# Optimization experiments

Measured on AMD Instinct MI355X. Metric: run time of the kernel, lower is better.

The kernel has to match this reference:

```python
import jax, jax.numpy as jnp
import numpy as np

DEPTH = 4
HEADS = 8
DIM = 512
HID = 1024  # int(512 * 2.0)
P = 16
IMG = 224
GRID = IMG // P          # 14
NPATCH = GRID * GRID     # 196
NTOK = NPATCH + 1        # 197 (cls token)
BATCH = 64
EPS = 1e-5               # torch LayerNorm default


def layernorm(x, w, b):
    mu = jnp.mean(x, axis=-1, keepdims=True)
    var = jnp.mean(jnp.square(x - mu), axis=-1, keepdims=True)
    return (x - mu) * jax.lax.rsqrt(var + EPS) * w + b


def setup_inputs() -> dict:
    key = jax.random.key(0)
    ks = jax.random.split(key, 12)
    s = 0.02
    inp = {
        "x": jax.random.normal(ks[0], (BATCH, 3, IMG, IMG), jnp.float32),
        # patch-embed conv as matmul: kernel flattened in torch order (c, kh, kw)
        "conv_w": jax.random.normal(ks[1], (3 * P * P, DIM), jnp.float32) * s,
        "conv_b": jnp.zeros((DIM,), jnp.float32),
        "cls_token": jax.random.normal(ks[2], (1, 1, DIM), jnp.float32) * s,
        "pos_embed": jax.random.normal(ks[3], (1, NTOK, DIM), jnp.float32) * s,
        # per-block params stacked along depth
        "ln1_w": jnp.ones((DEPTH, DIM), jnp.float32),
        "ln1_b": jnp.zeros((DEPTH, DIM), jnp.float32),
        "qkv_w": jax.random.normal(ks[4], (DEPTH, DIM, 3 * DIM), jnp.float32) * s,
        "qkv_b": jnp.zeros((DEPTH, 3 * DIM), jnp.float32),
        "proj_w": jax.random.normal(ks[5], (DEPTH, DIM, DIM), jnp.float32) * s,
        "proj_b": jnp.zeros((DEPTH, DIM), jnp.float32),
        "ln2_w": jnp.ones((DEPTH, DIM), jnp.float32),
        "ln2_b": jnp.zeros((DEPTH, DIM), jnp.float32),
        "fc1_w": jax.random.normal(ks[6], (DEPTH, DIM, HID), jnp.float32) * s,
        "fc1_b": jnp.zeros((DEPTH, HID), jnp.float32),
        "fc2_w": jax.random.normal(ks[7], (DEPTH, HID, DIM), jnp.float32) * s,
        "fc2_b": jnp.zeros((DEPTH, DIM), jnp.float32),
        "norm_w": jnp.ones((DIM,), jnp.float32),
        "norm_b": jnp.zeros((DIM,), jnp.float32),
    }
    return inp


def reference(x, conv_w, conv_b, cls_token, pos_embed,
              ln1_w, ln1_b, qkv_w, qkv_b, proj_w, proj_b,
              ln2_w, ln2_b, fc1_w, fc1_b, fc2_w, fc2_b,
              norm_w, norm_b):
    B = x.shape[0]
    hd = DIM // HEADS
    scale = hd ** -0.5
    # PatchEmbed: conv with kernel=stride=patch == patch extraction + matmul
    patches = x.reshape(B, 3, GRID, P, GRID, P)
    patches = patches.transpose(0, 2, 4, 1, 3, 5).reshape(B, NPATCH, 3 * P * P)
    tok = patches @ conv_w + conv_b                      # [B, 196, DIM]
    cls = jnp.broadcast_to(cls_token, (B, 1, DIM))
    h = jnp.concatenate([cls, tok], axis=1) + pos_embed  # [B, 197, DIM]
    for i in range(DEPTH):
        # Attention block (eval mode: dropouts are identity)
        y = layernorm(h, ln1_w[i], ln1_b[i])
        qkv = (y @ qkv_w[i] + qkv_b[i]).reshape(B, NTOK, 3, HEADS, hd)
        qkv = qkv.transpose(2, 0, 3, 1, 4)               # [3, B, H, N, hd]
        q, k, v = qkv[0], qkv[1], qkv[2]
        attn = jax.nn.softmax(jnp.einsum('bhnd,bhmd->bhnm', q, k) * scale, axis=-1)
        o = jnp.einsum('bhnm,bhmd->bhnd', attn, v)
        o = o.transpose(0, 2, 1, 3).reshape(B, NTOK, DIM)
        h = h + (o @ proj_w[i] + proj_b[i])
        # MLP block (exact GELU as in torch nn.GELU)
        y = layernorm(h, ln2_w[i], ln2_b[i])
        y = jax.nn.gelu(y @ fc1_w[i] + fc1_b[i], approximate=False)
        h = h + (y @ fc2_w[i] + fc2_b[i])
    return layernorm(h, norm_w, norm_b)
```

## Files before the change

### kernel.cpp

```cpp
#include <hip/hip_runtime.h>
#include <hip/hip_bf16.h>

#define HEADS 8
#define DIM 512
#define HID 1024
#define NTOK 197
#define NPATCH 196
#define BATCH 64
#define MTOK (BATCH*NTOK)
#define MPATCH (BATCH*NPATCH)
#define KPATCH 768

typedef __attribute__((ext_vector_type(8))) short vbf8;
typedef __attribute__((ext_vector_type(4))) float vf4;

__device__ inline float bf2f(short u) {
  union { unsigned int i; float f; } v; v.i = ((unsigned int)(unsigned short)u) << 16; return v.f;
}
__device__ inline short f2bf(float f) {
  union { float f; unsigned int i; } u; u.f = f;
  unsigned int r = u.i + 0x7fffu + ((u.i >> 16) & 1u);
  return (short)(r >> 16);
}

__device__ inline void gl_lds16(const void* g, void* l) {
  __builtin_amdgcn_global_load_lds(
      (const __attribute__((address_space(1))) void*)g,
      (__attribute__((address_space(3))) void*)l, 16, 0, 0);
}

__global__ void k_cvt_t(const float* __restrict__ in, short* __restrict__ out, int K, int N) {
  int slice = blockIdx.z;
  in  += (size_t)slice * K * N;
  out += (size_t)slice * K * N;
  __shared__ short tile[64][72];
  int t = threadIdx.x;
  int k0 = blockIdx.y * 64, n0 = blockIdx.x * 64;
  int r = t >> 2, c4 = (t & 3) << 4;
  #pragma unroll
  for (int j = 0; j < 16; j += 4) {
    float4 v = *(const float4*)(in + (size_t)(k0 + r) * N + n0 + c4 + j);
    tile[r][c4 + j + 0] = f2bf(v.x);
    tile[r][c4 + j + 1] = f2bf(v.y);
    tile[r][c4 + j + 2] = f2bf(v.z);
    tile[r][c4 + j + 3] = f2bf(v.w);
  }
  __syncthreads();
  int n = t >> 2, kc = (t & 3) << 4;
  vbf8 a, b;
  #pragma unroll
  for (int j = 0; j < 8; ++j) a[j] = tile[kc + j][n];
  #pragma unroll
  for (int j = 0; j < 8; ++j) b[j] = tile[kc + 8 + j][n];
  *(vbf8*)(out + (size_t)(n0 + n) * K + k0 + kc) = a;
  *(vbf8*)(out + (size_t)(n0 + n) * K + k0 + kc + 8) = b;
}

__global__ void k_im2col(const float* __restrict__ x, short* __restrict__ patches) {
  int tid = blockIdx.x * 256 + threadIdx.x;
  if (tid >= MPATCH * 48) return;
  int b = tid / (NPATCH * 48);
  int r = tid % (NPATCH * 48);
  int p = r / 48;
  int ck = r % 48;
  int c = ck >> 4, kh = ck & 15;
  int gy = p / 14, gx = p % 14;
  const float* src = x + ((size_t)((b * 3 + c) * 224) + gy * 16 + kh) * 224 + gx * 16;
  short* dst = patches + (size_t)(b * NPATCH + p) * KPATCH + c * 256 + kh * 16;
  float4 v0 = *(const float4*)(src);
  float4 v1 = *(const float4*)(src + 4);
  float4 v2 = *(const float4*)(src + 8);
  float4 v3 = *(const float4*)(src + 12);
  vbf8 o0, o1;
  o0[0]=f2bf(v0.x); o0[1]=f2bf(v0.y); o0[2]=f2bf(v0.z); o0[3]=f2bf(v0.w);
  o0[4]=f2bf(v1.x); o0[5]=f2bf(v1.y); o0[6]=f2bf(v1.z); o0[7]=f2bf(v1.w);
  o1[0]=f2bf(v2.x); o1[1]=f2bf(v2.y); o1[2]=f2bf(v2.z); o1[3]=f2bf(v2.w);
  o1[4]=f2bf(v3.x); o1[5]=f2bf(v3.y); o1[6]=f2bf(v3.z); o1[7]=f2bf(v3.w);
  *(vbf8*)dst = o0;
  *(vbf8*)(dst + 8) = o1;
}

__global__ void k_cls(const float* __restrict__ cls, const float* __restrict__ pos,
                      float* __restrict__ h) {
  int b = blockIdx.x, t = threadIdx.x;
  float* hr = h + (size_t)b * NTOK * DIM;
  hr[t]       = cls[t]       + pos[t];
  hr[t + 256] = cls[t + 256] + pos[t + 256];
}

template<int OUTBF>
__global__ __launch_bounds__(256) void k_ln(const float* __restrict__ x,
                                            const float* __restrict__ w,
                                            const float* __restrict__ b,
                                            void* __restrict__ out) {
  int wid = threadIdx.x >> 6, lane = threadIdx.x & 63;
  int row = blockIdx.x * 4 + wid;
  const float* xr = x + (size_t)row * DIM + lane * 8;
  float4 va = *(const float4*)xr;
  float4 vb = *(const float4*)(xr + 4);
  float s  = va.x + va.y + va.z + va.w + vb.x + vb.y + vb.z + vb.w;
  float ss = va.x*va.x + va.y*va.y + va.z*va.z + va.w*va.w
           + vb.x*vb.x + vb.y*vb.y + vb.z*vb.z + vb.w*vb.w;
  #pragma unroll
  for (int o = 32; o > 0; o >>= 1) { s += __shfl_xor(s, o); ss += __shfl_xor(ss, o); }
  float mu = s * (1.0f / DIM);
  float var = ss * (1.0f / DIM) - mu * mu;
  float rs = rsqrtf(var + 1e-5f);
  float4 wa = *(const float4*)(w + lane * 8);
  float4 wb = *(const float4*)(w + lane * 8 + 4);
  float4 ba = *(const float4*)(b + lane * 8);
  float4 bb = *(const float4*)(b + lane * 8 + 4);
  float y0 = (va.x - mu) * rs * wa.x + ba.x;
  float y1 = (va.y - mu) * rs * wa.y + ba.y;
  float y2 = (va.z - mu) * rs * wa.z + ba.z;
  float y3 = (va.w - mu) * rs * wa.w + ba.w;
  float y4 = (vb.x - mu) * rs * wb.x + bb.x;
  float y5 = (vb.y - mu) * rs * wb.y + bb.y;
  float y6 = (vb.z - mu) * rs * wb.z + bb.z;
  float y7 = (vb.w - mu) * rs * wb.w + bb.w;
  if (OUTBF) {
    vbf8 pk;
    pk[0]=f2bf(y0); pk[1]=f2bf(y1); pk[2]=f2bf(y2); pk[3]=f2bf(y3);
    pk[4]=f2bf(y4); pk[5]=f2bf(y5); pk[6]=f2bf(y6); pk[7]=f2bf(y7);
    *(vbf8*)((short*)out + (size_t)row * DIM + lane * 8) = pk;
  } else {
    float4 oa, ob;
    oa.x=y0; oa.y=y1; oa.z=y2; oa.w=y3;
    ob.x=y4; ob.y=y5; ob.z=y6; ob.w=y7;
    float* op = (float*)out + (size_t)row * DIM + lane * 8;
    *(float4*)op = oa;
    *(float4*)(op + 4) = ob;
  }
}

template<int MODE, int MF>
__global__ __launch_bounds__(256) void k_gemm(
    const short* __restrict__ A, const short* __restrict__ Bt,
    const float* __restrict__ bias, void* __restrict__ out,
    const float* __restrict__ extra, int M, int N, int K)
{
  constexpr int BM = MF * 32;
  __shared__ short As[BM * 64];
  __shared__ short Bs[128 * 64];
  int gx = gridDim.x;
  int nwg = gx * gridDim.y;
  int orig = blockIdx.y * gx + blockIdx.x;
  int q = nwg >> 3, r = nwg & 7, xcd = orig & 7, off = orig >> 3;
  int nid = (xcd < r ? xcd * (q + 1) : r * (q + 1) + (xcd - r) * q) + off;
  int bm = nid / gx, bn = nid % gx;

  int t = threadIdx.x, wid = t >> 6, lane = t & 63;
  int wm = wid >> 1, wn = wid & 1;
  int lr = lane & 15, lk = lane >> 4;

  const size_t lane_off = (size_t)(lane & 7) * K + (lane >> 3) * 8;
  const short* Abase = A  + (size_t)(bm * BM)  * K + lane_off;
  const short* Bbase = Bt + (size_t)(bn * 128) * K + lane_off;

  const int rdoff = (lr >> 3) * 512 + lk * 64 + (lr & 7) * 8;

  vf4 acc[MF][4];
  #pragma unroll
  for (int i = 0; i < MF; ++i)
    #pragma unroll
    for (int j = 0; j < 4; ++j) {
      acc[i][j][0] = 0.f; acc[i][j][1] = 0.f; acc[i][j][2] = 0.f; acc[i][j][3] = 0.f;
    }

  for (int k0 = 0; k0 < K; k0 += 64) {
    if (k0) __syncthreads();
    #pragma unroll
    for (int i = 0; i < MF; ++i) {
      int rc = wid * MF + i;
      gl_lds16(Abase + (size_t)(rc * 8) * K + k0, &As[rc * 512]);
    }
    #pragma unroll
    for (int i = 0; i < 4; ++i) {
      int rc = wid * 4 + i;
      gl_lds16(Bbase + (size_t)(rc * 8) * K + k0, &Bs[rc * 512]);
    }
    __syncthreads();
    #pragma unroll
    for (int s = 0; s < 2; ++s) {
      vbf8 af[MF], bfr[4];
      #pragma unroll
      for (int i = 0; i < MF; ++i)
        af[i] = *(const vbf8*)&As[(wm * (BM / 2) + i * 16) * 64 + s * 256 + rdoff];
      #pragma unroll
      for (int j = 0; j < 4; ++j)
        bfr[j] = *(const vbf8*)&Bs[(wn * 64 + j * 16) * 64 + s * 256 + rdoff];
      #pragma unroll
      for (int i = 0; i < MF; ++i)
        #pragma unroll
        for (int j = 0; j < 4; ++j)
          acc[i][j] = __builtin_amdgcn_mfma_f32_16x16x32_bf16(af[i], bfr[j], acc[i][j], 0, 0, 0);
    }
  }

  int rbase = bm * BM + wm * (BM / 2);
  int cbase = bn * 128 + wn * 64;
  #pragma unroll
  for (int i = 0; i < MF; ++i) {
    #pragma unroll
    for (int j = 0; j < 4; ++j) {
      int col = cbase + j * 16 + lr;
      float bs = bias[col];
      #pragma unroll
      for (int z = 0; z < 4; ++z) {
        int row = rbase + i * 16 + lk * 4 + z;
        if (row < M) {
          float v = acc[i][j][z] + bs;
          if (MODE == 0) {
            ((short*)out)[(size_t)row * N + col] = f2bf(v);
          } else if (MODE == 1) {
            float g = 0.5f * v * (1.f + erff(v * 0.70710678118f));
            ((short*)out)[(size_t)row * N + col] = f2bf(g);
          } else if (MODE == 2) {
            float* hp = (float*)out + (size_t)row * N + col;
            *hp = *hp + v;
          } else {
            int b_ = row / NPATCH, p = row - b_ * NPATCH;
            ((float*)out)[((size_t)b_ * NTOK + 1 + p) * DIM + col] =
                v + extra[(size_t)(1 + p) * DIM + col];
          }
        }
      }
    }
  }
}

#define VSTR 232
__global__ __launch_bounds__(256) void k_attn(const short* __restrict__ qkv,
                                              short* __restrict__ o) {
  int h = blockIdx.x, b = blockIdx.y;
  __shared__ short Vt[64 * VSTR];
  __shared__ short Pt[4][16 * VSTR];
  int t = threadIdx.x, wid = t >> 6, lane = t & 63;
  int lq = lane & 15, g4 = lane >> 4;
  const size_t base = (size_t)(b * NTOK) * 1536 + h * 64;

  vbf8 vz;
  #pragma unroll
  for (int j = 0; j < 8; ++j) vz[j] = 0;
  for (int idx = t; idx < 224 * 8; idx += 256) {
    int r = idx >> 3, c8 = idx & 7;
    vbf8 v = vz;
    if (r < NTOK) v = *(const vbf8*)(qkv + base + (size_t)r * 1536 + 1024 + c8 * 8);
    int cs = r ^ ((c8 & 3) << 3);
    #pragma unroll
    for (int j = 0; j < 8; ++j) Vt[(c8 * 8 + j) * VSTR + cs] = v[j];
  }
  __syncthreads();

  short* Pw = &Pt[wid][0];
  for (int qt = wid; qt < 13; qt += 4) {
    const short* qp = qkv + base + (size_t)(qt * 16 + lq) * 1536 + g4 * 8;
    vbf8 qf0 = *(const vbf8*)qp;
    vbf8 qf1 = *(const vbf8*)(qp + 32);
    float sc[13][4];
    #pragma unroll
    for (int kt = 0; kt < 13; ++kt) {
      const short* kp = qkv + base + (size_t)(kt * 16 + lq) * 1536 + 512 + g4 * 8;
      vbf8 kf0 = *(const vbf8*)kp;
      vbf8 kf1 = *(const vbf8*)(kp + 32);
      vf4 s; s[0] = 0.f; s[1] = 0.f; s[2] = 0.f; s[3] = 0.f;
      s = __builtin_amdgcn_mfma_f32_16x16x32_bf16(kf0, qf0, s, 0, 0, 0);
      s = __builtin_amdgcn_mfma_f32_16x16x32_bf16(kf1, qf1, s, 0, 0, 0);
      #pragma unroll
      for (int z = 0; z < 4; ++z) {
        int krow = kt * 16 + g4 * 4 + z;
        sc[kt][z] = (krow < NTOK) ? s[z] * 0.125f : -1e30f;
      }
    }
    float mx = -1e30f;
    #pragma unroll
    for (int kt = 0; kt < 13; ++kt)
      #pragma unroll
      for (int z = 0; z < 4; ++z) mx = fmaxf(mx, sc[kt][z]);
    mx = fmaxf(mx, __shfl_xor(mx, 16));
    mx = fmaxf(mx, __shfl_xor(mx, 32));
    float sum = 0.f;
    #pragma unroll
    for (int kt = 0; kt < 13; ++kt)
      #pragma unroll
      for (int z = 0; z < 4; ++z) {
        float e = __expf(sc[kt][z] - mx);
        sc[kt][z] = e;
        sum += e;
      }
    sum += __shfl_xor(sum, 16);
    sum += __shfl_xor(sum, 32);
    float inv = 1.f / sum;
    #pragma unroll
    for (int kt = 0; kt < 13; ++kt) {
      *(short4*)&Pw[lq * VSTR + kt * 16 + g4 * 4] =
          make_short4(f2bf(sc[kt][0]), f2bf(sc[kt][1]), f2bf(sc[kt][2]), f2bf(sc[kt][3]));
    }
    *(short4*)&Pw[lq * VSTR + 208 + g4 * 4] = make_short4(0, 0, 0, 0);
    vf4 oacc[4];
    #pragma unroll
    for (int dt = 0; dt < 4; ++dt) { oacc[dt][0]=0.f; oacc[dt][1]=0.f; oacc[dt][2]=0.f; oacc[dt][3]=0.f; }
    #pragma unroll
    for (int u = 0; u < 7; ++u) {
      vbf8 pb = *(const vbf8*)&Pw[lq * VSTR + u * 32 + g4 * 8];
      #pragma unroll
      for (int dt = 0; dt < 4; ++dt) {
        int swz = ((dt * 2 + (lq >> 3)) & 3) << 3;
        vbf8 va = *(const vbf8*)&Vt[(dt * 16 + lq) * VSTR + ((u * 32 + g4 * 8) ^ swz)];
        oacc[dt] = __builtin_amdgcn_mfma_f32_16x16x32_bf16(va, pb, oacc[dt], 0, 0, 0);
      }
    }
    int qrow = qt * 16 + lq;
    if (qrow < NTOK) {
      short* op = o + ((size_t)(b * NTOK) + qrow) * DIM + h * 64 + g4 * 4;
      #pragma unroll
      for (int dt = 0; dt < 4; ++dt)
        *(short4*)(op + dt * 16) = make_short4(f2bf(oacc[dt][0] * inv), f2bf(oacc[dt][1] * inv),
                                               f2bf(oacc[dt][2] * inv), f2bf(oacc[dt][3] * inv));
    }
  }
}

extern "C" void kernel_launch(void* const* d_in, const int* in_sizes, int n_in,
                              void* d_out, int out_size, void* d_ws, size_t ws_size,
                              hipStream_t stream) {
  (void)in_sizes; (void)n_in; (void)out_size; (void)ws_size;
  const float* x      = (const float*)d_in[0];
  const float* conv_w = (const float*)d_in[1];
  const float* conv_b = (const float*)d_in[2];
  const float* cls    = (const float*)d_in[3];
  const float* pos    = (const float*)d_in[4];
  const float* ln1_w  = (const float*)d_in[5];
  const float* ln1_b  = (const float*)d_in[6];
  const float* qkv_w  = (const float*)d_in[7];
  const float* qkv_b  = (const float*)d_in[8];
  const float* proj_w = (const float*)d_in[9];
  const float* proj_b = (const float*)d_in[10];
  const float* ln2_w  = (const float*)d_in[11];
  const float* ln2_b  = (const float*)d_in[12];
  const float* fc1_w  = (const float*)d_in[13];
  const float* fc1_b  = (const float*)d_in[14];
  const float* fc2_w  = (const float*)d_in[15];
  const float* fc2_b  = (const float*)d_in[16];
  const float* norm_w = (const float*)d_in[17];
  const float* norm_b = (const float*)d_in[18];

  short* conv_wT = (short*)d_ws;
  short* qkv_wT  = conv_wT + (size_t)512 * 768;
  short* proj_wT = qkv_wT  + (size_t)4 * 1536 * 512;
  short* fc1_wT  = proj_wT + (size_t)4 * 512 * 512;
  short* fc2_wT  = fc1_wT  + (size_t)4 * 512 * 1024;
  short* y_bf    = fc2_wT  + (size_t)4 * 1024 * 512;
  short* o_bf    = y_bf    + (size_t)MTOK * 512;
  short* big     = o_bf    + (size_t)MTOK * 512;
  float* h       = (float*)(big + (size_t)MTOK * 1536);

  k_cvt_t<<<dim3(8, 12, 1), 256, 0, stream>>>(conv_w, conv_wT, 768, 512);
  k_cvt_t<<<dim3(24, 8, 4), 256, 0, stream>>>(qkv_w, qkv_wT, 512, 1536);
  k_cvt_t<<<dim3(8, 8, 4), 256, 0, stream>>>(proj_w, proj_wT, 512, 512);
  k_cvt_t<<<dim3(16, 8, 4), 256, 0, stream>>>(fc1_w, fc1_wT, 512, 1024);
  k_cvt_t<<<dim3(8, 16, 4), 256, 0, stream>>>(fc2_w, fc2_wT, 1024, 512);

  k_im2col<<<2352, 256, 0, stream>>>(x, big);
  k_cls<<<64, 256, 0, stream>>>(cls, pos, h);
  k_gemm<3, 2><<<dim3(4, 196), 256, 0, stream>>>(big, conv_wT, conv_b, h, pos,
                                                 MPATCH, 512, 768);
  for (int i = 0; i < 4; ++i) {
    k_ln<1><<<MTOK / 4, 256, 0, stream>>>(h, ln1_w + i * 512, ln1_b + i * 512, y_bf);
    k_gemm<0, 4><<<dim3(12, 99), 256, 0, stream>>>(y_bf, qkv_wT + (size_t)i * 512 * 1536,
                                                   qkv_b + i * 1536, big, nullptr,
                                                   MTOK, 1536, 512);
    k_attn<<<dim3(8, 64), 256, 0, stream>>>(big, o_bf);
    k_gemm<2, 2><<<dim3(4, 197), 256, 0, stream>>>(o_bf, proj_wT + (size_t)i * 512 * 512,
                                                   proj_b + i * 512, h, nullptr,
                                                   MTOK, 512, 512);
    k_ln<1><<<MTOK / 4, 256, 0, stream>>>(h, ln2_w + i * 512, ln2_b + i * 512, y_bf);
    k_gemm<1, 4><<<dim3(8, 99), 256, 0, stream>>>(y_bf, fc1_wT + (size_t)i * 512 * 1024,
                                                  fc1_b + i * 1024, big, nullptr,
                                                  MTOK, 1024, 512);
    k_gemm<2, 2><<<dim3(4, 197), 256, 0, stream>>>(big, fc2_wT + (size_t)i * 1024 * 512,
                                                   fc2_b + i * 512, h, nullptr,
                                                   MTOK, 512, 1024);
  }
  k_ln<0><<<MTOK / 4, 256, 0, stream>>>(h, norm_w, norm_b, d_out);
}
```

Baseline: 1.058 ms.

## Replace LDS-staged GEMM with direct-from-global MFMA operand loads and 128x128 tiles

Rewrites the GEMM kernel so each wave loads its MFMA operand fragments straight from global memory into registers, with no LDS staging and no barriers. All GEMMs now use a fixed 128x128 block tile, and the grids are adjusted to match. This removes the LDS round trip and the __syncthreads stalls. In exchange, operands are no longer shared across waves through LDS, so global and L2 traffic goes up. Each lane's 16-byte loads are strided by row, so coalescing is poor, and out-of-range rows on the last M tile may be read without guards.

```diff
diff --git a/kernel.cpp b/kernel.cpp
--- a/kernel.cpp
+++ b/kernel.cpp
@@ -21,12 +21,6 @@
   union { float f; unsigned int i; } u; u.f = f;
   unsigned int r = u.i + 0x7fffu + ((u.i >> 16) & 1u);
   return (short)(r >> 16);
-}
-
-__device__ inline void gl_lds16(const void* g, void* l) {
-  __builtin_amdgcn_global_load_lds(
-      (const __attribute__((address_space(1))) void*)g,
-      (__attribute__((address_space(3))) void*)l, 16, 0, 0);
 }
 
 __global__ void k_cvt_t(const float* __restrict__ in, short* __restrict__ out, int K, int N) {
@@ -133,15 +127,12 @@
   }
 }
 
-template<int MODE, int MF>
-__global__ __launch_bounds__(256) void k_gemm(
+template<int MODE>
+__global__ __launch_bounds__(256) void k_gemm_d(
     const short* __restrict__ A, const short* __restrict__ Bt,
     const float* __restrict__ bias, void* __restrict__ out,
     const float* __restrict__ extra, int M, int N, int K)
 {
-  constexpr int BM = MF * 32;
-  __shared__ short As[BM * 64];
-  __shared__ short Bs[128 * 64];
   int gx = gridDim.x;
   int nwg = gx * gridDim.y;
   int orig = blockIdx.y * gx + blockIdx.x;
@@ -153,54 +144,55 @@
   int wm = wid >> 1, wn = wid & 1;
   int lr = lane & 15, lk = lane >> 4;
 
-  const size_t lane_off = (size_t)(lane & 7) * K + (lane >> 3) * 8;
-  const short* Abase = A  + (size_t)(bm * BM)  * K + lane_off;
-  const short* Bbase = Bt + (size_t)(bn * 128) * K + lane_off;
-
-  const int rdoff = (lr >> 3) * 512 + lk * 64 + (lr & 7) * 8;
-
-  vf4 acc[MF][4];
-  #pragma unroll
-  for (int i = 0; i < MF; ++i)
+  const short* ar0 = A  + (size_t)(bm * 128 + wm * 64 +  0 + lr) * K + lk * 8;
+  const short* ar1 = ar0 + (size_t)16 * K;
+  const short* ar2 = ar0 + (size_t)32 * K;
+  const short* ar3 = ar0 + (size_t)48 * K;
+  const short* br0 = Bt + (size_t)(bn * 128 + wn * 64 +  0 + lr) * K + lk * 8;
+  const short* br1 = br0 + (size_t)16 * K;
+  const short* br2 = br0 + (size_t)32 * K;
+  const short* br3 = br0 + (size_t)48 * K;
+
+  vf4 acc[4][4];
+  #pragma unroll
+  for (int i = 0; i < 4; ++i)
     #pragma unroll
     for (int j = 0; j < 4; ++j) {
       acc[i][j][0] = 0.f; acc[i][j][1] = 0.f; acc[i][j][2] = 0.f; acc[i][j][3] = 0.f;
     }
 
-  for (int k0 = 0; k0 < K; k0 += 64) {
-    if (k0) __syncthreads();
-    #pragma unroll
-    for (int i = 0; i < MF; ++i) {
-      int rc = wid * MF + i;
-      gl_lds16(Abase + (size_t)(rc * 8) * K + k0, &As[rc * 512]);
-    }
-    #pragma unroll
-    for (int i = 0; i < 4; ++i) {
-      int rc = wid * 4 + i;
-      gl_lds16(Bbase + (size_t)(rc * 8) * K + k0, &Bs[rc * 512]);
-    }
-    __syncthreads();
-    #pragma unroll
-    for (int s = 0; s < 2; ++s) {
-      vbf8 af[MF], bfr[4];
-      #pragma unroll
-      for (int i = 0; i < MF; ++i)
-        af[i] = *(const vbf8*)&As[(wm * (BM / 2) + i * 16) * 64 + s * 256 + rdoff];
-      #pragma unroll
-      for (int j = 0; j < 4; ++j)
-        bfr[j] = *(const vbf8*)&Bs[(wn * 64 + j * 16) * 64 + s * 256 + rdoff];
-      #pragma unroll
-      for (int i = 0; i < MF; ++i)
-        #pragma unroll
-        for (int j = 0; j < 4; ++j)
-          acc[i][j] = __builtin_amdgcn_mfma_f32_16x16x32_bf16(af[i], bfr[j], acc[i][j], 0, 0, 0);
-    }
-  }
-
-  int rbase = bm * BM + wm * (BM / 2);
+  #pragma unroll 4
+  for (int k0 = 0; k0 < K; k0 += 32) {
+    vbf8 a0 = *(const vbf8*)(ar0 + k0);
+    vbf8 a1 = *(const vbf8*)(ar1 + k0);
+    vbf8 a2 = *(const vbf8*)(ar2 + k0);
+    vbf8 a3 = *(const vbf8*)(ar3 + k0);
+    vbf8 b0 = *(const vbf8*)(br0 + k0);
+    vbf8 b1 = *(const vbf8*)(br1 + k0);
+    vbf8 b2 = *(const vbf8*)(br2 + k0);
+    vbf8 b3 = *(const vbf8*)(br3 + k0);
+    acc[0][0] = __builtin_amdgcn_mfma_f32_16x16x32_bf16(a0, b0, acc[0][0], 0, 0, 0);
+    acc[0][1] = __builtin_amdgcn_mfma_f32_16x16x32_bf16(a0, b1, acc[0][1], 0, 0, 0);
+    acc[0][2] = __builtin_amdgcn_mfma_f32_16x16x32_bf16(a0, b2, acc[0][2], 0, 0, 0);
+    acc[0][3] = __builtin_amdgcn_mfma_f32_16x16x32_bf16(a0, b3, acc[0][3], 0, 0, 0);
+    acc[1][0] = __builtin_amdgcn_mfma_f32_16x16x32_bf16(a1, b0, acc[1][0], 0, 0, 0);
+    acc[1][1] = __builtin_amdgcn_mfma_f32_16x16x32_bf16(a1, b1, acc[1][1], 0, 0, 0);
+    acc[1][2] = __builtin_amdgcn_mfma_f32_16x16x32_bf16(a1, b2, acc[1][2], 0, 0, 0);
+    acc[1][3] = __builtin_amdgcn_mfma_f32_16x16x32_bf16(a1, b3, acc[1][3], 0, 0, 0);
+    acc[2][0] = __builtin_amdgcn_mfma_f32_16x16x32_bf16(a2, b0, acc[2][0], 0, 0, 0);
+    acc[2][1] = __builtin_amdgcn_mfma_f32_16x16x32_bf16(a2, b1, acc[2][1], 0, 0, 0);
+    acc[2][2] = __builtin_amdgcn_mfma_f32_16x16x32_bf16(a2, b2, acc[2][2], 0, 0, 0);
+    acc[2][3] = __builtin_amdgcn_mfma_f32_16x16x32_bf16(a2, b3, acc[2][3], 0, 0, 0);
+    acc[3][0] = __builtin_amdgcn_mfma_f32_16x16x32_bf16(a3, b0, acc[3][0], 0, 0, 0);
+    acc[3][1] = __builtin_amdgcn_mfma_f32_16x16x32_bf16(a3, b1, acc[3][1], 0, 0, 0);
+    acc[3][2] = __builtin_amdgcn_mfma_f32_16x16x32_bf16(a3, b2, acc[3][2], 0, 0, 0);
+    acc[3][3] = __builtin_amdgcn_mfma_f32_16x16x32_bf16(a3, b3, acc[3][3], 0, 0, 0);
+  }
+
+  int rbase = bm * 128 + wm * 64;
   int cbase = bn * 128 + wn * 64;
   #pragma unroll
-  for (int i = 0; i < MF; ++i) {
+  for (int i = 0; i < 4; ++i) {
     #pragma unroll
     for (int j = 0; j < 4; ++j) {
       int col = cbase + j * 16 + lr;
@@ -363,24 +355,24 @@
 
   k_im2col<<<2352, 256, 0, stream>>>(x, big);
   k_cls<<<64, 256, 0, stream>>>(cls, pos, h);
-  k_gemm<3, 2><<<dim3(4, 196), 256, 0, stream>>>(big, conv_wT, conv_b, h, pos,
-                                                 MPATCH, 512, 768);
+  k_gemm_d<3><<<dim3(4, 98), 256, 0, stream>>>(big, conv_wT, conv_b, h, pos,
+                                               MPATCH, 512, 768);
   for (int i = 0; i < 4; ++i) {
     k_ln<1><<<MTOK / 4, 256, 0, stream>>>(h, ln1_w + i * 512, ln1_b + i * 512, y_bf);
-    k_gemm<0, 4><<<dim3(12, 99), 256, 0, stream>>>(y_bf, qkv_wT + (size_t)i * 512 * 1536,
-                                                   qkv_b + i * 1536, big, nullptr,
-                                                   MTOK, 1536, 512);
+    k_gemm_d<0><<<dim3(12, 99), 256, 0, stream>>>(y_bf, qkv_wT + (size_t)i * 512 * 1536,
+                                                  qkv_b + i * 1536, big, nullptr,
+                                                  MTOK, 1536, 512);
     k_attn<<<dim3(8, 64), 256, 0, stream>>>(big, o_bf);
-    k_gemm<2, 2><<<dim3(4, 197), 256, 0, stream>>>(o_bf, proj_wT + (size_t)i * 512 * 512,
-                                                   proj_b + i * 512, h, nullptr,
-                                                   MTOK, 512, 512);
+    k_gemm_d<2><<<dim3(4, 99), 256, 0, stream>>>(o_bf, proj_wT + (size_t)i * 512 * 512,
+                                                 proj_b + i * 512, h, nullptr,
+                                                 MTOK, 512, 512);
     k_ln<1><<<MTOK / 4, 256, 0, stream>>>(h, ln2_w + i * 512, ln2_b + i * 512, y_bf);
-    k_gemm<1, 4><<<dim3(8, 99), 256, 0, stream>>>(y_bf, fc1_wT + (size_t)i * 512 * 1024,
-                                                  fc1_b + i * 1024, big, nullptr,
-                                                  MTOK, 1024, 512);
-    k_gemm<2, 2><<<dim3(4, 197), 256, 0, stream>>>(big, fc2_wT + (size_t)i * 1024 * 512,
-                                                   fc2_b + i * 512, h, nullptr,
-                                                   MTOK, 512, 1024);
+    k_gemm_d<1><<<dim3(8, 99), 256, 0, stream>>>(y_bf, fc1_wT + (size_t)i * 512 * 1024,
+                                                 fc1_b + i * 1024, big, nullptr,
+                                                 MTOK, 1024, 512);
+    k_gemm_d<2><<<dim3(4, 99), 256, 0, stream>>>(big, fc2_wT + (size_t)i * 1024 * 512,
+                                                 fc2_b + i * 512, h, nullptr,
+                                                 MTOK, 512, 1024);
   }
   k_ln<0><<<MTOK / 4, 256, 0, stream>>>(h, norm_w, norm_b, d_out);
 }
```

Result: slower. 1.425 ms (+34.7%).

## Use 128x128 GEMM tiles everywhere with split-K atomics for N=512 GEMMs

Applied to the files above, without the earlier changes.

Unifies all GEMMs on a 128x128 block tile and, for the narrow N=512 GEMMs (patch embed, proj, fc2), splits K across two blocks that accumulate into the fp32 residual with atomicAdd. Bias and pos-embed for patch tokens are pre-initialized by a new init kernel so the patch GEMM only adds its partial sums. The goal is more MFMA reuse per tile while keeping enough blocks in flight. The cost is atomic traffic on h and a nondeterministic summation order.

```diff
diff --git a/kernel.cpp b/kernel.cpp
--- a/kernel.cpp
+++ b/kernel.cpp
@@ -80,12 +80,14 @@
   *(vbf8*)(dst + 8) = o1;
 }
 
-__global__ void k_cls(const float* __restrict__ cls, const float* __restrict__ pos,
-                      float* __restrict__ h) {
-  int b = blockIdx.x, t = threadIdx.x;
-  float* hr = h + (size_t)b * NTOK * DIM;
-  hr[t]       = cls[t]       + pos[t];
-  hr[t + 256] = cls[t + 256] + pos[t + 256];
+__global__ void k_init(const float* __restrict__ cls, const float* __restrict__ pos,
+                       const float* __restrict__ conv_b, float* __restrict__ h) {
+  int tok = blockIdx.x, b = blockIdx.y, t = threadIdx.x;
+  float* hr = h + ((size_t)b * NTOK + tok) * DIM;
+  const float* pr = pos + (size_t)tok * DIM;
+  const float* ad = (tok == 0) ? cls : conv_b;
+  hr[t]       = ad[t]       + pr[t];
+  hr[t + 256] = ad[t + 256] + pr[t + 256];
 }
 
 template<int OUTBF>
@@ -133,14 +135,13 @@
   }
 }
 
-template<int MODE, int MF>
+template<int MODE, int KS>
 __global__ __launch_bounds__(256) void k_gemm(
     const short* __restrict__ A, const short* __restrict__ Bt,
     const float* __restrict__ bias, void* __restrict__ out,
-    const float* __restrict__ extra, int M, int N, int K)
+    int M, int N, int K)
 {
-  constexpr int BM = MF * 32;
-  __shared__ short As[BM * 64];
+  __shared__ short As[128 * 64];
   __shared__ short Bs[128 * 64];
   int gx = gridDim.x;
   int nwg = gx * gridDim.y;
@@ -148,59 +149,56 @@
   int q = nwg >> 3, r = nwg & 7, xcd = orig & 7, off = orig >> 3;
   int nid = (xcd < r ? xcd * (q + 1) : r * (q + 1) + (xcd - r) * q) + off;
   int bm = nid / gx, bn = nid % gx;
+  int ks = blockIdx.z;
 
   int t = threadIdx.x, wid = t >> 6, lane = t & 63;
   int wm = wid >> 1, wn = wid & 1;
   int lr = lane & 15, lk = lane >> 4;
 
   const size_t lane_off = (size_t)(lane & 7) * K + (lane >> 3) * 8;
-  const short* Abase = A  + (size_t)(bm * BM)  * K + lane_off;
+  const short* Abase = A  + (size_t)(bm * 128) * K + lane_off;
   const short* Bbase = Bt + (size_t)(bn * 128) * K + lane_off;
-
   const int rdoff = (lr >> 3) * 512 + lk * 64 + (lr & 7) * 8;
 
-  vf4 acc[MF][4];
-  #pragma unroll
-  for (int i = 0; i < MF; ++i)
+  vf4 acc[4][4];
+  #pragma unroll
+  for (int i = 0; i < 4; ++i)
     #pragma unroll
     for (int j = 0; j < 4; ++j) {
       acc[i][j][0] = 0.f; acc[i][j][1] = 0.f; acc[i][j][2] = 0.f; acc[i][j][3] = 0.f;
     }
 
-  for (int k0 = 0; k0 < K; k0 += 64) {
-    if (k0) __syncthreads();
-    #pragma unroll
-    for (int i = 0; i < MF; ++i) {
-      int rc = wid * MF + i;
-      gl_lds16(Abase + (size_t)(rc * 8) * K + k0, &As[rc * 512]);
-    }
+  const int kbeg = ks * (K / KS), kend = kbeg + K / KS;
+  for (int k0 = kbeg; k0 < kend; k0 += 64) {
+    if (k0 != kbeg) __syncthreads();
     #pragma unroll
     for (int i = 0; i < 4; ++i) {
       int rc = wid * 4 + i;
+      gl_lds16(Abase + (size_t)(rc * 8) * K + k0, &As[rc * 512]);
       gl_lds16(Bbase + (size_t)(rc * 8) * K + k0, &Bs[rc * 512]);
     }
     __syncthreads();
     #pragma unroll
     for (int s = 0; s < 2; ++s) {
-      vbf8 af[MF], bfr[4];
-      #pragma unroll
-      for (int i = 0; i < MF; ++i)
-        af[i] = *(const vbf8*)&As[(wm * (BM / 2) + i * 16) * 64 + s * 256 + rdoff];
+      vbf8 af[4], bfr[4];
+      #pragma unroll
+      for (int i = 0; i < 4; ++i)
+        af[i] = *(const vbf8*)&As[(wm * 64 + i * 16) * 64 + s * 256 + rdoff];
       #pragma unroll
       for (int j = 0; j < 4; ++j)
         bfr[j] = *(const vbf8*)&Bs[(wn * 64 + j * 16) * 64 + s * 256 + rdoff];
       #pragma unroll
-      for (int i = 0; i < MF; ++i)
+      for (int i = 0; i < 4; ++i)
         #pragma unroll
         for (int j = 0; j < 4; ++j)
           acc[i][j] = __builtin_amdgcn_mfma_f32_16x16x32_bf16(af[i], bfr[j], acc[i][j], 0, 0, 0);
     }
   }
 
-  int rbase = bm * BM + wm * (BM / 2);
+  int rbase = bm * 128 + wm * 64;
   int cbase = bn * 128 + wn * 64;
   #pragma unroll
-  for (int i = 0; i < MF; ++i) {
+  for (int i = 0; i < 4; ++i) {
     #pragma unroll
     for (int j = 0; j < 4; ++j) {
       int col = cbase + j * 16 + lr;
@@ -209,19 +207,19 @@
       for (int z = 0; z < 4; ++z) {
         int row = rbase + i * 16 + lk * 4 + z;
         if (row < M) {
-          float v = acc[i][j][z] + bs;
           if (MODE == 0) {
-            ((short*)out)[(size_t)row * N + col] = f2bf(v);
+            ((short*)out)[(size_t)row * N + col] = f2bf(acc[i][j][z] + bs);
           } else if (MODE == 1) {
+            float v = acc[i][j][z] + bs;
             float g = 0.5f * v * (1.f + erff(v * 0.70710678118f));
             ((short*)out)[(size_t)row * N + col] = f2bf(g);
           } else if (MODE == 2) {
-            float* hp = (float*)out + (size_t)row * N + col;
-            *hp = *hp + v;
+            float v = acc[i][j][z] + ((KS == 1 || ks == 0) ? bs : 0.f);
+            atomicAdd((float*)out + (size_t)row * N + col, v);
           } else {
             int b_ = row / NPATCH, p = row - b_ * NPATCH;
-            ((float*)out)[((size_t)b_ * NTOK + 1 + p) * DIM + col] =
-                v + extra[(size_t)(1 + p) * DIM + col];
+            atomicAdd(&((float*)out)[((size_t)b_ * NTOK + 1 + p) * DIM + col],
+                      acc[i][j][z]);
           }
         }
       }
@@ -362,25 +360,25 @@
   k_cvt_t<<<dim3(8, 16, 4), 256, 0, stream>>>(fc2_w, fc2_wT, 1024, 512);
 
   k_im2col<<<2352, 256, 0, stream>>>(x, big);
-  k_cls<<<64, 256, 0, stream>>>(cls, pos, h);
-  k_gemm<3, 2><<<dim3(4, 196), 256, 0, stream>>>(big, conv_wT, conv_b, h, pos,
-                                                 MPATCH, 512, 768);
+  k_init<<<dim3(197, 64), 256, 0, stream>>>(cls, pos, conv_b, h);
+  k_gemm<3, 2><<<dim3(4, 98, 2), 256, 0, stream>>>(big, conv_wT, conv_b, h,
+                                                   MPATCH, 512, 768);
   for (int i = 0; i < 4; ++i) {
     k_ln<1><<<MTOK / 4, 256, 0, stream>>>(h, ln1_w + i * 512, ln1_b + i * 512, y_bf);
-    k_gemm<0, 4><<<dim3(12, 99), 256, 0, stream>>>(y_bf, qkv_wT + (size_t)i * 512 * 1536,
-                                                   qkv_b + i * 1536, big, nullptr,
+    k_gemm<0, 1><<<dim3(12, 99), 256, 0, stream>>>(y_bf, qkv_wT + (size_t)i * 512 * 1536,
+                                                   qkv_b + i * 1536, big,
                                                    MTOK, 1536, 512);
     k_attn<<<dim3(8, 64), 256, 0, stream>>>(big, o_bf);
-    k_gemm<2, 2><<<dim3(4, 197), 256, 0, stream>>>(o_bf, proj_wT + (size_t)i * 512 * 512,
-                                                   proj_b + i * 512, h, nullptr,
-                                                   MTOK, 512, 512);
+    k_gemm<2, 2><<<dim3(4, 99, 2), 256, 0, stream>>>(o_bf, proj_wT + (size_t)i * 512 * 512,
+                                                     proj_b + i * 512, h,
+                                                     MTOK, 512, 512);
     k_ln<1><<<MTOK / 4, 256, 0, stream>>>(h, ln2_w + i * 512, ln2_b + i * 512, y_bf);
-    k_gemm<1, 4><<<dim3(8, 99), 256, 0, stream>>>(y_bf, fc1_wT + (size_t)i * 512 * 1024,
-                                                  fc1_b + i * 1024, big, nullptr,
+    k_gemm<1, 1><<<dim3(8, 99), 256, 0, stream>>>(y_bf, fc1_wT + (size_t)i * 512 * 1024,
+                                                  fc1_b + i * 1024, big,
                                                   MTOK, 1024, 512);
-    k_gemm<2, 2><<<dim3(4, 197), 256, 0, stream>>>(big, fc2_wT + (size_t)i * 1024 * 512,
-                                                   fc2_b + i * 512, h, nullptr,
-                                                   MTOK, 512, 1024);
+    k_gemm<2, 2><<<dim3(4, 99, 2), 256, 0, stream>>>(big, fc2_wT + (size_t)i * 1024 * 512,
+                                                     fc2_b + i * 512, h,
+                                                     MTOK, 512, 1024);
   }
   k_ln<0><<<MTOK / 4, 256, 0, stream>>>(h, norm_w, norm_b, d_out);
 }
```

Measured after the change: 1.220 ms. 1.15x slower.

## Use uniform 128x128 GEMM tiles with multi-step K staging per barrier

Applied to the files above, without the earlier changes.

Every GEMM now uses a fixed 128x128 tile with a 4x4 MFMA accumulator block per wave, instead of a height chosen per call. A KU template parameter stages several 64-wide K slices in LDS per barrier, so the conv, proj and fc2 GEMMs sync half as often. The XCD-aware block remapping is dropped, and the LDS layout becomes plain row-major. Larger tiles halve the grid for the 512-wide GEMMs, which may underfill the GPU. The row-major LDS reads may also cause bank conflicts that the old interleaved layout avoided.

```diff
diff --git a/kernel.cpp b/kernel.cpp
--- a/kernel.cpp
+++ b/kernel.cpp
@@ -133,74 +133,67 @@
   }
 }
 
-template<int MODE, int MF>
+template<int MODE, int KU>
 __global__ __launch_bounds__(256) void k_gemm(
     const short* __restrict__ A, const short* __restrict__ Bt,
     const float* __restrict__ bias, void* __restrict__ out,
     const float* __restrict__ extra, int M, int N, int K)
 {
-  constexpr int BM = MF * 32;
-  __shared__ short As[BM * 64];
-  __shared__ short Bs[128 * 64];
-  int gx = gridDim.x;
-  int nwg = gx * gridDim.y;
-  int orig = blockIdx.y * gx + blockIdx.x;
-  int q = nwg >> 3, r = nwg & 7, xcd = orig & 7, off = orig >> 3;
-  int nid = (xcd < r ? xcd * (q + 1) : r * (q + 1) + (xcd - r) * q) + off;
-  int bm = nid / gx, bn = nid % gx;
-
+  __shared__ short As[KU][128 * 64];
+  __shared__ short Bs[KU][128 * 64];
+  int bn = blockIdx.x, bm = blockIdx.y;
   int t = threadIdx.x, wid = t >> 6, lane = t & 63;
   int wm = wid >> 1, wn = wid & 1;
   int lr = lane & 15, lk = lane >> 4;
-
-  const size_t lane_off = (size_t)(lane & 7) * K + (lane >> 3) * 8;
-  const short* Abase = A  + (size_t)(bm * BM)  * K + lane_off;
-  const short* Bbase = Bt + (size_t)(bn * 128) * K + lane_off;
-
-  const int rdoff = (lr >> 3) * 512 + lk * 64 + (lr & 7) * 8;
-
-  vf4 acc[MF][4];
-  #pragma unroll
-  for (int i = 0; i < MF; ++i)
+  int srow = lane >> 3;
+  int scol = (lane & 7) * 8;
+  vf4 acc[4][4];
+  #pragma unroll
+  for (int i = 0; i < 4; ++i)
     #pragma unroll
     for (int j = 0; j < 4; ++j) {
       acc[i][j][0] = 0.f; acc[i][j][1] = 0.f; acc[i][j][2] = 0.f; acc[i][j][3] = 0.f;
     }
 
-  for (int k0 = 0; k0 < K; k0 += 64) {
+  const short* Abase = A  + (size_t)(bm * 128 + srow) * K + scol;
+  const short* Bbase = Bt + (size_t)(bn * 128 + srow) * K + scol;
+
+  for (int k0 = 0; k0 < K; k0 += KU * 64) {
     if (k0) __syncthreads();
     #pragma unroll
-    for (int i = 0; i < MF; ++i) {
-      int rc = wid * MF + i;
-      gl_lds16(Abase + (size_t)(rc * 8) * K + k0, &As[rc * 512]);
-    }
-    #pragma unroll
-    for (int i = 0; i < 4; ++i) {
-      int rc = wid * 4 + i;
-      gl_lds16(Bbase + (size_t)(rc * 8) * K + k0, &Bs[rc * 512]);
+    for (int u = 0; u < KU; ++u) {
+      #pragma unroll
+      for (int i = 0; i < 4; ++i) {
+        int rc = wid * 4 + i;
+        gl_lds16(Abase + (size_t)(rc * 8) * K + k0 + u * 64, &As[u][rc * 512]);
+        gl_lds16(Bbase + (size_t)(rc * 8) * K + k0 + u * 64, &Bs[u][rc * 512]);
+      }
     }
     __syncthreads();
     #pragma unroll
-    for (int s = 0; s < 2; ++s) {
-      vbf8 af[MF], bfr[4];
-      #pragma unroll
-      for (int i = 0; i < MF; ++i)
-        af[i] = *(const vbf8*)&As[(wm * (BM / 2) + i * 16) * 64 + s * 256 + rdoff];
-      #pragma unroll
-      for (int j = 0; j < 4; ++j)
-        bfr[j] = *(const vbf8*)&Bs[(wn * 64 + j * 16) * 64 + s * 256 + rdoff];
-      #pragma unroll
-      for (int i = 0; i < MF; ++i)
+    for (int u = 0; u < KU; ++u) {
+      #pragma unroll
+      for (int s = 0; s < 2; ++s) {
+        vbf8 af[4], bfr[4];
+        #pragma unroll
+        for (int i = 0; i < 4; ++i)
+          af[i] = *(const vbf8*)&As[u][(wm * 64 + i * 16 + lr) * 64 + s * 32 + lk * 8];
         #pragma unroll
         for (int j = 0; j < 4; ++j)
-          acc[i][j] = __builtin_amdgcn_mfma_f32_16x16x32_bf16(af[i], bfr[j], acc[i][j], 0, 0, 0);
-    }
-  }
-
-  int rbase = bm * BM + wm * (BM / 2);
+          bfr[j] = *(const vbf8*)&Bs[u][(wn * 64 + j * 16 + lr) * 64 + s * 32 + lk * 8];
+        #pragma unroll
+        for (int i = 0; i < 4; ++i)
+          #pragma unroll
+          for (int j = 0; j < 4; ++j)
+            acc[i][j] = __builtin_amdgcn_mfma_f32_16x16x32_bf16(af[i], bfr[j], acc[i][j], 0, 0, 0);
+      }
+    }
+  }
+
+  int rbase = bm * 128 + wm * 64;
   int cbase = bn * 128 + wn * 64;
   #pragma unroll
-  for (int i = 0; i < MF; ++i) {
+  for (int i = 0; i < 4; ++i) {
     #pragma unroll
     for (int j = 0; j < 4; ++j) {
       int col = cbase + j * 16 + lr;
@@ -363,24 +356,24 @@
 
   k_im2col<<<2352, 256, 0, stream>>>(x, big);
   k_cls<<<64, 256, 0, stream>>>(cls, pos, h);
-  k_gemm<3, 2><<<dim3(4, 196), 256, 0, stream>>>(big, conv_wT, conv_b, h, pos,
-                                                 MPATCH, 512, 768);
+  k_gemm<3, 2><<<dim3(4, 98), 256, 0, stream>>>(big, conv_wT, conv_b, h, pos,
+                                                MPATCH, 512, 768);
   for (int i = 0; i < 4; ++i) {
     k_ln<1><<<MTOK / 4, 256, 0, stream>>>(h, ln1_w + i * 512, ln1_b + i * 512, y_bf);
-    k_gemm<0, 4><<<dim3(12, 99), 256, 0, stream>>>(y_bf, qkv_wT + (size_t)i * 512 * 1536,
+    k_gemm<0, 1><<<dim3(12, 99), 256, 0, stream>>>(y_bf, qkv_wT + (size_t)i * 512 * 1536,
                                                    qkv_b + i * 1536, big, nullptr,
                                                    MTOK, 1536, 512);
     k_attn<<<dim3(8, 64), 256, 0, stream>>>(big, o_bf);
-    k_gemm<2, 2><<<dim3(4, 197), 256, 0, stream>>>(o_bf, proj_wT + (size_t)i * 512 * 512,
-                                                   proj_b + i * 512, h, nullptr,
-                                                   MTOK, 512, 512);
+    k_gemm<2, 2><<<dim3(4, 99), 256, 0, stream>>>(o_bf, proj_wT + (size_t)i * 512 * 512,
+                                                  proj_b + i * 512, h, nullptr,
+                                                  MTOK, 512, 512);
     k_ln<1><<<MTOK / 4, 256, 0, stream>>>(h, ln2_w + i * 512, ln2_b + i * 512, y_bf);
-    k_gemm<1, 4><<<dim3(8, 99), 256, 0, stream>>>(y_bf, fc1_wT + (size_t)i * 512 * 1024,
+    k_gemm<1, 1><<<dim3(8, 99), 256, 0, stream>>>(y_bf, fc1_wT + (size_t)i * 512 * 1024,
                                                   fc1_b + i * 1024, big, nullptr,
                                                   MTOK, 1024, 512);
-    k_gemm<2, 2><<<dim3(4, 197), 256, 0, stream>>>(big, fc2_wT + (size_t)i * 1024 * 512,
-                                                   fc2_b + i * 512, h, nullptr,
-                                                   MTOK, 512, 1024);
+    k_gemm<2, 2><<<dim3(4, 99), 256, 0, stream>>>(big, fc2_wT + (size_t)i * 1024 * 512,
+                                                  fc2_b + i * 512, h, nullptr,
+                                                  MTOK, 512, 1024);
   }
   k_ln<0><<<MTOK / 4, 256, 0, stream>>>(h, norm_w, norm_b, d_out);
 }
```

New measurement: 893.7 us. 1.18x faster.
